# Kernel optimization log

Hardware: AMD Instinct MI355X
Metric: run time of the kernel (lower is better)

## Reference

```python
import jax, jax.numpy as jnp
import numpy as np

N_X, N_NEIGH, D_IN, D_HID, D_OUT = 8192, 8192, 512, 32, 256
NEG_BIG = -9.0e15


def setup_inputs() -> dict:
    key = jax.random.key(0)
    ks = jax.random.split(key, 16)
    s_in = 1.0 / np.sqrt(D_IN)
    s_hid = 1.0 / np.sqrt(D_HID)
    return {
        "x": jax.random.normal(ks[0], (N_X, D_IN), jnp.float32),
        "neigh": jax.random.normal(ks[1], (N_NEIGH, D_IN), jnp.float32),
        "adj": jax.random.randint(ks[2], (N_X, N_NEIGH), 0, 2, jnp.int32),
        # att_x MLP: Linear(D_IN,D_HID) -> tanh -> Linear(D_HID,D_HID)
        "Wx1": jax.random.uniform(ks[3], (D_IN, D_HID), jnp.float32, -s_in, s_in),
        "bx1": jnp.zeros((D_HID,), jnp.float32),
        "Wx2": jax.random.uniform(ks[4], (D_HID, D_HID), jnp.float32, -s_hid, s_hid),
        "bx2": jnp.zeros((D_HID,), jnp.float32),
        # att_neigh MLP
        "Wn1": jax.random.uniform(ks[5], (D_IN, D_HID), jnp.float32, -s_in, s_in),
        "bn1": jnp.zeros((D_HID,), jnp.float32),
        "Wn2": jax.random.uniform(ks[6], (D_HID, D_HID), jnp.float32, -s_hid, s_hid),
        "bn2": jnp.zeros((D_HID,), jnp.float32),
        # fc_value, fc_x
        "Wv": jax.random.uniform(ks[7], (D_IN, D_OUT), jnp.float32, -s_in, s_in),
        "bv": jnp.zeros((D_OUT,), jnp.float32),
        "Wfx": jax.random.uniform(ks[8], (D_IN, D_OUT), jnp.float32, -s_in, s_in),
        "bfx": jnp.zeros((D_OUT,), jnp.float32),
    }


def reference(x, neigh, adj, Wx1, bx1, Wx2, bx2, Wn1, bn1, Wn2, bn2, Wv, bv, Wfx, bfx):
    # eval mode: dropouts are identity. edge_emb gather in original is dead code.
    neib_att = jnp.tanh(neigh @ Wn1 + bn1) @ Wn2 + bn2      # (N_neigh, H)
    value = neigh @ Wv + bv                                  # (N_neigh, D_OUT)
    x_att = jnp.tanh(x @ Wx1 + bx1) @ Wx2 + bx2              # (N_x, H)
    ws = jnp.einsum("nh,mh->nm", x_att, neib_att)            # (N_x, N_neigh)
    ws = jax.nn.leaky_relu(ws, negative_slope=0.01)
    ws = jnp.where(adj > 0, ws, jnp.float32(NEG_BIG))
    ws = jax.nn.softmax(ws, axis=1)
    agg_neib = ws @ value                                    # (N_x, D_OUT)
    out = jnp.concatenate([x @ Wfx + bfx, agg_neib], axis=1)  # (N_x, 2*D_OUT)
    return out
```

## Files before the change

### kernel.cpp

```cpp
#include <hip/hip_runtime.h>
#include <hip/hip_bf16.h>

#define NX 8192
#define NN 8192
#define DIN 512
#define DHID 32
#define DOUT 256

typedef __bf16 bf16x8 __attribute__((ext_vector_type(8)));
typedef float f32x4 __attribute__((ext_vector_type(4)));
typedef unsigned short u16x8 __attribute__((ext_vector_type(8)));

__device__ __forceinline__ unsigned short f2bf(float f) {
  __hip_bfloat16 h = __float2bfloat16(f);
  return __builtin_bit_cast(unsigned short, h);
}
__device__ __forceinline__ float bf2f(unsigned short u) {
  unsigned int v = ((unsigned int)u) << 16;
  return __builtin_bit_cast(float, v);
}
__device__ __forceinline__ f32x4 mfma16(u16x8 a, u16x8 b, f32x4 c) {
  return __builtin_amdgcn_mfma_f32_16x16x32_bf16(
      __builtin_bit_cast(bf16x8, a), __builtin_bit_cast(bf16x8, b), c, 0, 0, 0);
}
__device__ __forceinline__ u16x8 cvt8(float4 a0, float4 a1) {
  u16x8 u;
  u[0] = f2bf(a0.x); u[1] = f2bf(a0.y); u[2] = f2bf(a0.z); u[3] = f2bf(a0.w);
  u[4] = f2bf(a1.x); u[5] = f2bf(a1.y); u[6] = f2bf(a1.z); u[7] = f2bf(a1.w);
  return u;
}

__global__ __launch_bounds__(256) void k_wt(
    const float* __restrict__ Wv, const float* __restrict__ Wfx,
    const float* __restrict__ Wx1, const float* __restrict__ Wn1,
    const float* __restrict__ Wx2, const float* __restrict__ Wn2,
    unsigned short* __restrict__ WvT, unsigned short* __restrict__ WfxT,
    unsigned short* __restrict__ Wx1T, unsigned short* __restrict__ Wn1T,
    unsigned short* __restrict__ Wx2T, unsigned short* __restrict__ Wn2T) {
  const float* src; unsigned short* dst; int K, C;
  switch (blockIdx.y) {
    case 0:  src = Wv;  dst = WvT;  K = DIN; C = 256; break;
    case 1:  src = Wfx; dst = WfxT; K = DIN; C = 256; break;
    case 2:  src = Wx1; dst = Wx1T; K = DIN; C = 32;  break;
    case 3:  src = Wn1; dst = Wn1T; K = DIN; C = 32;  break;
    case 4:  src = Wx2; dst = Wx2T; K = 32;  C = 32;  break;
    default: src = Wn2; dst = Wn2T; K = 32;  C = 32;  break;
  }
  int tc = C >> 5, tk = K >> 5;
  if ((int)blockIdx.x >= tc * tk) return;
  int ik = blockIdx.x / tc, ic = blockIdx.x % tc;
  __shared__ float tile[32][33];
  int t = threadIdx.x, tx = t & 31, ty0 = t >> 5;
  #pragma unroll
  for (int q = 0; q < 4; ++q) {
    int ty = ty0 + q * 8;
    tile[ty][tx] = src[(ik * 32 + ty) * C + ic * 32 + tx];
  }
  __syncthreads();
  #pragma unroll
  for (int q = 0; q < 4; ++q) {
    int ty = ty0 + q * 8;
    dst[(ic * 32 + ty) * K + ik * 32 + tx] = f2bf(tile[tx][ty]);
  }
}

__global__ __launch_bounds__(256) void k_prep(
    const float* __restrict__ x, const float* __restrict__ neigh,
    const float* __restrict__ bfx, const float* __restrict__ bv,
    const float* __restrict__ bx1, const float* __restrict__ bn1,
    const unsigned short* __restrict__ WfxT, const unsigned short* __restrict__ WvT,
    const unsigned short* __restrict__ Wx1T, const unsigned short* __restrict__ Wn1T,
    float* __restrict__ out, unsigned short* __restrict__ Vp,
    unsigned short* __restrict__ Hx, unsigned short* __restrict__ Hn) {
  int job = blockIdx.y;
  const float* A = job ? neigh : x;
  const float* bias = job ? bv : bfx;
  const float* b1 = job ? bn1 : bx1;
  const unsigned short* WT = job ? WvT : WfxT;
  const unsigned short* W1T = job ? Wn1T : Wx1T;
  unsigned short* H = job ? Hn : Hx;
  __shared__ __align__(16) char As[2][64 * 64];
  int t = threadIdx.x;
  int lane = t & 63, w = t >> 6;
  int r = lane & 15, h4 = lane >> 4;
  int bm = blockIdx.x * 64;
  f32x4 acc[4][4];
  f32x4 acch[4];
  #pragma unroll
  for (int i = 0; i < 4; ++i) {
    acch[i] = (f32x4){0.f, 0.f, 0.f, 0.f};
    #pragma unroll
    for (int j = 0; j < 4; ++j) acc[i][j] = (f32x4){0.f, 0.f, 0.f, 0.f};
  }
  int srow = t >> 2, kq = t & 3;
  const float* ap = A + (long)(bm + srow) * DIN + kq * 8;
  float4 a0 = *reinterpret_cast<const float4*>(ap);
  float4 a1 = *reinterpret_cast<const float4*>(ap + 4);
  u16x8 pbc[4], pbhc;
  #pragma unroll
  for (int nt = 0; nt < 4; ++nt)
    pbc[nt] = *reinterpret_cast<const u16x8*>(WT + (w * 64 + nt * 16 + r) * DIN + h4 * 8);
  if (w < 2)
    pbhc = *reinterpret_cast<const u16x8*>(W1T + (w * 16 + r) * DIN + h4 * 8);
  int boff = (srow * 64 + kq * 16) ^ ((srow & 3) << 4);
  int buf = 0;
  for (int kk = 0; kk < 16; ++kk) {
    u16x8 u = cvt8(a0, a1);
    *reinterpret_cast<u16x8*>(&As[buf][0] + boff) = u;
    __syncthreads();
    u16x8 pbn[4], pbhn;
    if (kk < 15) {
      a0 = *reinterpret_cast<const float4*>(ap + (kk + 1) * 32);
      a1 = *reinterpret_cast<const float4*>(ap + (kk + 1) * 32 + 4);
      #pragma unroll
      for (int nt = 0; nt < 4; ++nt)
        pbn[nt] = *reinterpret_cast<const u16x8*>(
            WT + (w * 64 + nt * 16 + r) * DIN + (kk + 1) * 32 + h4 * 8);
      if (w < 2)
        pbhn = *reinterpret_cast<const u16x8*>(
            W1T + (w * 16 + r) * DIN + (kk + 1) * 32 + h4 * 8);
    }
    #pragma unroll
    for (int mt = 0; mt < 4; ++mt) {
      int ro = mt * 16 + r;
      int aoff = (ro * 64 + h4 * 16) ^ ((ro & 3) << 4);
      u16x8 pa = *reinterpret_cast<const u16x8*>(&As[buf][0] + aoff);
      #pragma unroll
      for (int nt = 0; nt < 4; ++nt) acc[mt][nt] = mfma16(pa, pbc[nt], acc[mt][nt]);
      if (w < 2) acch[mt] = mfma16(pa, pbhc, acch[mt]);
    }
    #pragma unroll
    for (int nt = 0; nt < 4; ++nt) pbc[nt] = pbn[nt];
    pbhc = pbhn;
    buf ^= 1;
  }
  #pragma unroll
  for (int mt = 0; mt < 4; ++mt)
    #pragma unroll
    for (int nt = 0; nt < 4; ++nt) {
      int c = w * 64 + nt * 16 + r;
      #pragma unroll
      for (int j = 0; j < 4; ++j) {
        int row = bm + mt * 16 + h4 * 4 + j;
        float v = acc[mt][nt][j] + bias[c];
        if (job == 0) out[(long)row * 512 + c] = v;
        else Vp[((row >> 3) * 256 + c) * 8 + (row & 7)] = f2bf(v);
      }
    }
  if (w < 2) {
    int c = w * 16 + r;
    float bb = b1[c];
    #pragma unroll
    for (int mt = 0; mt < 4; ++mt)
      #pragma unroll
      for (int j = 0; j < 4; ++j) {
        int row = bm + mt * 16 + h4 * 4 + j;
        H[row * DHID + c] = f2bf(tanhf(acch[mt][j] + bb));
      }
  }
}

__global__ __launch_bounds__(256) void k_att(
    const unsigned short* __restrict__ Hx, const unsigned short* __restrict__ Hn,
    const float* __restrict__ bx2, const float* __restrict__ bn2,
    const unsigned short* __restrict__ Wx2T, const unsigned short* __restrict__ Wn2T,
    unsigned short* __restrict__ xatt, unsigned short* __restrict__ natt) {
  const unsigned short* H; const float* b2; const unsigned short* WT; unsigned short* att;
  if (blockIdx.y == 0) { H = Hx; b2 = bx2; WT = Wx2T; att = xatt; }
  else                 { H = Hn; b2 = bn2; WT = Wn2T; att = natt; }
  int lane = threadIdx.x & 63, w = threadIdx.x >> 6;
  int r = lane & 15, h4 = lane >> 4;
  int row = blockIdx.x * 64 + w * 16 + r;
  u16x8 af = *reinterpret_cast<const u16x8*>(H + row * DHID + h4 * 8);
  u16x8 b0 = *reinterpret_cast<const u16x8*>(WT + r * DHID + h4 * 8);
  u16x8 b1 = *reinterpret_cast<const u16x8*>(WT + (16 + r) * DHID + h4 * 8);
  f32x4 z = {0.f, 0.f, 0.f, 0.f};
  f32x4 acc0 = mfma16(af, b0, z);
  f32x4 acc1 = mfma16(af, b1, z);
  int orow = blockIdx.x * 64 + w * 16 + h4 * 4;
  #pragma unroll
  for (int j = 0; j < 4; ++j) {
    att[(orow + j) * DHID + r]      = f2bf(acc0[j] + b2[r]);
    att[(orow + j) * DHID + 16 + r] = f2bf(acc1[j] + b2[16 + r]);
  }
}

__global__ __launch_bounds__(256, 4) void k_flash(
    const int* __restrict__ adj, const unsigned short* __restrict__ xatt,
    const unsigned short* __restrict__ natt, const unsigned short* __restrict__ Vp,
    float* __restrict__ out, unsigned short* __restrict__ accP,
    float* __restrict__ lP, int nc) {
  __shared__ unsigned short P[2][32 * 72];
  __shared__ float lpart[4][32];
  int t = threadIdx.x;
  int lane = t & 63, w = t >> 6;
  int r = lane & 15, h4 = lane >> 4;
  int rb = blockIdx.x * 32;
  int L = NN / nc;
  int base = blockIdx.y * L;
  int NIT = L / 64;
  u16x8 qf0 = *reinterpret_cast<const u16x8*>(xatt + (rb + r) * DHID + h4 * 8);
  u16x8 qf1 = *reinterpret_cast<const u16x8*>(xatt + (rb + 16 + r) * DHID + h4 * 8);
  f32x4 o[2][4];
  #pragma unroll
  for (int i = 0; i < 2; ++i)
    #pragma unroll
    for (int j = 0; j < 4; ++j) o[i][j] = (f32x4){0.f, 0.f, 0.f, 0.f};
  float psum[8];
  #pragma unroll
  for (int i = 0; i < 8; ++i) psum[i] = 0.f;
  int adjA[8], adjB[8];
  u16x8 kfA, kfB;
  long arow = (long)rb * NN + w * 16 + r;
  #pragma unroll
  for (int rt = 0; rt < 2; ++rt)
    #pragma unroll
    for (int j = 0; j < 4; ++j) {
      long ro = (long)(rt * 16 + h4 * 4 + j) * NN;
      adjA[rt * 4 + j] = adj[arow + ro + base];
      adjB[rt * 4 + j] = adj[arow + ro + base + 64];
    }
  kfA = *reinterpret_cast<const u16x8*>(natt + (base + w * 16 + r) * DHID + h4 * 8);
  kfB = *reinterpret_cast<const u16x8*>(natt + (base + 64 + w * 16 + r) * DHID + h4 * 8);
  int buf = 0;
  int lastn = base + L - 64;
  for (int it = 0; it < NIT; ++it) {
    int n0 = base + it * 64;
    f32x4 z = {0.f, 0.f, 0.f, 0.f};
    f32x4 s0 = mfma16(qf0, kfA, z);
    f32x4 s1 = mfma16(qf1, kfA, z);
    unsigned short* Pb = &P[buf][0];
    #pragma unroll
    for (int rt = 0; rt < 2; ++rt) {
      f32x4 s = rt ? s1 : s0;
      #pragma unroll
      for (int j = 0; j < 4; ++j) {
        float sv = s[j];
        float lr = fminf(fmaxf(sv, 0.01f * sv), 60.f);
        float p = (adjA[rt * 4 + j] > 0) ? __expf(lr) : 0.f;
        psum[rt * 4 + j] += p;
        Pb[(rt * 16 + h4 * 4 + j) * 72 + w * 16 + r] = f2bf(p);
      }
    }
    __syncthreads();
    #pragma unroll
    for (int q = 0; q < 8; ++q) adjA[q] = adjB[q];
    kfA = kfB;
    int n2 = n0 + 128 <= lastn ? n0 + 128 : lastn;
    #pragma unroll
    for (int rt = 0; rt < 2; ++rt)
      #pragma unroll
      for (int j = 0; j < 4; ++j)
        adjB[rt * 4 + j] = adj[arow + (long)(rt * 16 + h4 * 4 + j) * NN + n2];
    kfB = *reinterpret_cast<const u16x8*>(natt + (n2 + w * 16 + r) * DHID + h4 * 8);
    u16x8 pa[2][2], vf[2][4];
    #pragma unroll
    for (int kb = 0; kb < 2; ++kb) {
      pa[kb][0] = *reinterpret_cast<const u16x8*>(Pb + r * 72 + kb * 32 + h4 * 8);
      pa[kb][1] = *reinterpret_cast<const u16x8*>(Pb + (16 + r) * 72 + kb * 32 + h4 * 8);
    }
    #pragma unroll
    for (int kb = 0; kb < 2; ++kb) {
      long vbase = ((long)((n0 + kb * 32) >> 3) + h4) * (DOUT * 8);
      #pragma unroll
      for (int nt = 0; nt < 4; ++nt)
        vf[kb][nt] = *reinterpret_cast<const u16x8*>(Vp + vbase + (w * 64 + nt * 16 + r) * 8);
    }
    #pragma unroll
    for (int kb = 0; kb < 2; ++kb)
      #pragma unroll
      for (int nt = 0; nt < 4; ++nt) {
        o[0][nt] = mfma16(pa[kb][0], vf[kb][nt], o[0][nt]);
        o[1][nt] = mfma16(pa[kb][1], vf[kb][nt], o[1][nt]);
      }
    buf ^= 1;
  }
  #pragma unroll
  for (int q = 1; q < 16; q <<= 1)
    #pragma unroll
    for (int i = 0; i < 8; ++i) psum[i] += __shfl_xor(psum[i], q);
  if (r == 0) {
    #pragma unroll
    for (int rt = 0; rt < 2; ++rt)
      #pragma unroll
      for (int j = 0; j < 4; ++j)
        lpart[w][rt * 16 + h4 * 4 + j] = psum[rt * 4 + j];
  }
  __syncthreads();
  if (nc == 1) {
    #pragma unroll
    for (int rt = 0; rt < 2; ++rt)
      #pragma unroll
      for (int nt = 0; nt < 4; ++nt) {
        int c = w * 64 + nt * 16 + r;
        #pragma unroll
        for (int j = 0; j < 4; ++j) {
          int rl = rt * 16 + h4 * 4 + j;
          float l = lpart[0][rl] + lpart[1][rl] + lpart[2][rl] + lpart[3][rl];
          out[(long)(rb + rl) * 512 + 256 + c] = o[rt][nt][j] / l;
        }
      }
  } else {
    long cb = (long)blockIdx.y * NX;
    #pragma unroll
    for (int rt = 0; rt < 2; ++rt)
      #pragma unroll
      for (int nt = 0; nt < 4; ++nt) {
        int c = w * 64 + nt * 16 + r;
        #pragma unroll
        for (int j = 0; j < 4; ++j) {
          int rl = rt * 16 + h4 * 4 + j;
          accP[(cb + rb + rl) * DOUT + c] = f2bf(o[rt][nt][j]);
        }
      }
    if (t < 32)
      lP[blockIdx.y * NX + rb + t] =
          lpart[0][t] + lpart[1][t] + lpart[2][t] + lpart[3][t];
  }
}

__global__ __launch_bounds__(256) void k_combine(
    const unsigned short* __restrict__ accP, const float* __restrict__ lP,
    float* __restrict__ out, int nc) {
  long idx = (long)blockIdx.x * 256 + threadIdx.x;
  int row = (int)(idx >> 8), c = (int)(idx & 255);
  float s = 0.f, l = 0.f;
  for (int q = 0; q < nc; ++q) {
    s += bf2f(accP[(long)q * NX * DOUT + idx]);
    l += lP[q * NX + row];
  }
  out[(long)row * 512 + 256 + c] = s / l;
}

extern "C" void kernel_launch(void* const* d_in, const int* in_sizes, int n_in,
                              void* d_out, int out_size, void* d_ws, size_t ws_size,
                              hipStream_t stream) {
  const float* x    = (const float*)d_in[0];
  const float* neigh= (const float*)d_in[1];
  const int*   adj  = (const int*)d_in[2];
  const float* Wx1  = (const float*)d_in[3];
  const float* bx1  = (const float*)d_in[4];
  const float* Wx2  = (const float*)d_in[5];
  const float* bx2  = (const float*)d_in[6];
  const float* Wn1  = (const float*)d_in[7];
  const float* bn1  = (const float*)d_in[8];
  const float* Wn2  = (const float*)d_in[9];
  const float* bn2  = (const float*)d_in[10];
  const float* Wv   = (const float*)d_in[11];
  const float* bv   = (const float*)d_in[12];
  const float* Wfx  = (const float*)d_in[13];
  const float* bfx  = (const float*)d_in[14];
  float* out = (float*)d_out;
  char* ws = (char*)d_ws;

  unsigned short* xatt = (unsigned short*)(ws + 0);
  unsigned short* natt = (unsigned short*)(ws + 524288);
  unsigned short* Hx   = (unsigned short*)(ws + 1048576);
  unsigned short* Hn   = (unsigned short*)(ws + 1572864);
  unsigned short* Vp   = (unsigned short*)(ws + 2097152);
  unsigned short* WvT  = (unsigned short*)(ws + 6291456);
  unsigned short* WfxT = (unsigned short*)(ws + 6553600);
  unsigned short* Wx1T = (unsigned short*)(ws + 6815744);
  unsigned short* Wn1T = (unsigned short*)(ws + 6848512);
  unsigned short* Wx2T = (unsigned short*)(ws + 6881280);
  unsigned short* Wn2T = (unsigned short*)(ws + 6883328);

  const size_t OFF_ACC = 7340032;
  const size_t CHUNK_ACC = (size_t)NX * DOUT * 2;
  size_t need4 = OFF_ACC + 4 * (CHUNK_ACC + (size_t)NX * 4);
  size_t need2 = OFF_ACC + 2 * (CHUNK_ACC + (size_t)NX * 4);
  int nc = (ws_size >= need4) ? 4 : (ws_size >= need2) ? 2 : 1;
  unsigned short* accP = (unsigned short*)(ws + OFF_ACC);
  float* lP = (float*)(ws + OFF_ACC + (size_t)nc * CHUNK_ACC);

  k_wt<<<dim3(128, 6), 256, 0, stream>>>(Wv, Wfx, Wx1, Wn1, Wx2, Wn2,
                                         WvT, WfxT, Wx1T, Wn1T, Wx2T, Wn2T);
  k_prep<<<dim3(128, 2), 256, 0, stream>>>(x, neigh, bfx, bv, bx1, bn1,
                                           WfxT, WvT, Wx1T, Wn1T, out, Vp, Hx, Hn);
  k_att<<<dim3(128, 2), 256, 0, stream>>>(Hx, Hn, bx2, bn2, Wx2T, Wn2T, xatt, natt);
  k_flash<<<dim3(256, nc), 256, 0, stream>>>(adj, xatt, natt, Vp, out, accP, lP, nc);
  if (nc > 1)
    k_combine<<<dim3(NX * DOUT / 256), 256, 0, stream>>>(accP, lP, out, nc);
}
```

Measured before the change: 496.8 us.

## Pack adjacency into bitmask in separate pass before flash kernel

Adds a k_pack kernel that streams the int32 adjacency matrix once with nontemporal loads and ballots it into a 1-bit-per-edge mask. The flash kernel then reads 32-bit mask words and tests a per-lane bit instead of loading one int per element. The aim is to take the heavy strided adjacency reads out of the compute-bound attention loop and shrink that loop's memory footprint 32x. The cost is an extra kernel launch and a full read of adj in the pack pass, plus more workspace, which moves OFF_ACC and so can lower the split count nc if the workspace is small.

```diff
diff --git a/kernel.cpp b/kernel.cpp
--- a/kernel.cpp
+++ b/kernel.cpp
@@ -6,6 +6,7 @@
 #define DIN 512
 #define DHID 32
 #define DOUT 256
+#define NPW (NN / 32)
 
 typedef __bf16 bf16x8 __attribute__((ext_vector_type(8)));
 typedef float f32x4 __attribute__((ext_vector_type(4)));
@@ -61,6 +62,24 @@
   for (int q = 0; q < 4; ++q) {
     int ty = ty0 + q * 8;
     dst[(ic * 32 + ty) * K + ik * 32 + tx] = f2bf(tile[tx][ty]);
+  }
+}
+
+__global__ __launch_bounds__(256) void k_pack(
+    const int* __restrict__ adj, unsigned int* __restrict__ pack) {
+  long total = (long)NX * NN;
+  int gw = (blockIdx.x * 256 + threadIdx.x) >> 6;
+  int lane = threadIdx.x & 63;
+  int nw = (gridDim.x * 256) >> 6;
+  for (long s = (long)gw * 128; s < total; s += (long)nw * 128) {
+    int a0 = __builtin_nontemporal_load(&adj[s + lane]);
+    int a1 = __builtin_nontemporal_load(&adj[s + 64 + lane]);
+    unsigned long long b0 = __ballot(a0 > 0);
+    unsigned long long b1 = __ballot(a1 > 0);
+    if (lane == 0) {
+      *reinterpret_cast<unsigned long long*>(&pack[s >> 5]) = b0;
+      *reinterpret_cast<unsigned long long*>(&pack[(s >> 5) + 2]) = b1;
+    }
   }
 }
 
@@ -186,7 +205,7 @@
 }
 
 __global__ __launch_bounds__(256, 4) void k_flash(
-    const int* __restrict__ adj, const unsigned short* __restrict__ xatt,
+    const unsigned int* __restrict__ pack, const unsigned short* __restrict__ xatt,
     const unsigned short* __restrict__ natt, const unsigned short* __restrict__ Vp,
     float* __restrict__ out, unsigned short* __restrict__ accP,
     float* __restrict__ lP, int nc) {
@@ -209,16 +228,17 @@
   float psum[8];
   #pragma unroll
   for (int i = 0; i < 8; ++i) psum[i] = 0.f;
-  int adjA[8], adjB[8];
+  unsigned int bmask = 1u << (((w & 1) << 4) + r);
+  int wofs = w >> 1;
+  unsigned int mA[8], mB[8];
   u16x8 kfA, kfB;
-  long arow = (long)rb * NN + w * 16 + r;
   #pragma unroll
   for (int rt = 0; rt < 2; ++rt)
     #pragma unroll
     for (int j = 0; j < 4; ++j) {
-      long ro = (long)(rt * 16 + h4 * 4 + j) * NN;
-      adjA[rt * 4 + j] = adj[arow + ro + base];
-      adjB[rt * 4 + j] = adj[arow + ro + base + 64];
+      long prow = (long)(rb + rt * 16 + h4 * 4 + j) * NPW;
+      mA[rt * 4 + j] = __builtin_nontemporal_load(&pack[prow + (base >> 5) + wofs]);
+      mB[rt * 4 + j] = __builtin_nontemporal_load(&pack[prow + ((base + 64) >> 5) + wofs]);
     }
   kfA = *reinterpret_cast<const u16x8*>(natt + (base + w * 16 + r) * DHID + h4 * 8);
   kfB = *reinterpret_cast<const u16x8*>(natt + (base + 64 + w * 16 + r) * DHID + h4 * 8);
@@ -237,21 +257,22 @@
       for (int j = 0; j < 4; ++j) {
         float sv = s[j];
         float lr = fminf(fmaxf(sv, 0.01f * sv), 60.f);
-        float p = (adjA[rt * 4 + j] > 0) ? __expf(lr) : 0.f;
+        float p = (mA[rt * 4 + j] & bmask) ? __expf(lr) : 0.f;
         psum[rt * 4 + j] += p;
         Pb[(rt * 16 + h4 * 4 + j) * 72 + w * 16 + r] = f2bf(p);
       }
     }
     __syncthreads();
     #pragma unroll
-    for (int q = 0; q < 8; ++q) adjA[q] = adjB[q];
+    for (int q = 0; q < 8; ++q) mA[q] = mB[q];
     kfA = kfB;
     int n2 = n0 + 128 <= lastn ? n0 + 128 : lastn;
     #pragma unroll
     for (int rt = 0; rt < 2; ++rt)
       #pragma unroll
       for (int j = 0; j < 4; ++j)
-        adjB[rt * 4 + j] = adj[arow + (long)(rt * 16 + h4 * 4 + j) * NN + n2];
+        mB[rt * 4 + j] = __builtin_nontemporal_load(
+            &pack[(long)(rb + rt * 16 + h4 * 4 + j) * NPW + (n2 >> 5) + wofs]);
     kfB = *reinterpret_cast<const u16x8*>(natt + (n2 + w * 16 + r) * DHID + h4 * 8);
     u16x8 pa[2][2], vf[2][4];
     #pragma unroll
@@ -364,8 +385,9 @@
   unsigned short* Wn1T = (unsigned short*)(ws + 6848512);
   unsigned short* Wx2T = (unsigned short*)(ws + 6881280);
   unsigned short* Wn2T = (unsigned short*)(ws + 6883328);
-
-  const size_t OFF_ACC = 7340032;
+  unsigned int*   packb = (unsigned int*)(ws + 7340032);
+
+  const size_t OFF_ACC = 16777216;
   const size_t CHUNK_ACC = (size_t)NX * DOUT * 2;
   size_t need4 = OFF_ACC + 4 * (CHUNK_ACC + (size_t)NX * 4);
   size_t need2 = OFF_ACC + 2 * (CHUNK_ACC + (size_t)NX * 4);
@@ -375,10 +397,11 @@
 
   k_wt<<<dim3(128, 6), 256, 0, stream>>>(Wv, Wfx, Wx1, Wn1, Wx2, Wn2,
                                          WvT, WfxT, Wx1T, Wn1T, Wx2T, Wn2T);
+  k_pack<<<dim3(2048), 256, 0, stream>>>(adj, packb);
   k_prep<<<dim3(128, 2), 256, 0, stream>>>(x, neigh, bfx, bv, bx1, bn1,
                                            WfxT, WvT, Wx1T, Wn1T, out, Vp, Hx, Hn);
   k_att<<<dim3(128, 2), 256, 0, stream>>>(Hx, Hn, bx2, bn2, Wx2T, Wn2T, xatt, natt);
-  k_flash<<<dim3(256, nc), 256, 0, stream>>>(adj, xatt, natt, Vp, out, accP, lP, nc);
+  k_flash<<<dim3(256, nc), 256, 0, stream>>>(packb, xatt, natt, Vp, out, accP, lP, nc);
   if (nc > 1)
     k_combine<<<dim3(NX * DOUT / 256), 256, 0, stream>>>(accP, lP, out, nc);
 }
```

Measured after the change: 529.8 us. 6.6% more time.
